# Kernel tuning notes

Measured on AMD Instinct MI355X. Metric: run time of the kernel, lower is better.

Reference implementation:

```python
import jax, jax.numpy as jnp
import numpy as np

B, SQ, SK, TT, DM, H, HKV, D, FF = 1, 2048, 3072, 4096, 2048, 16, 8, 128, 6144
EPS = 1e-6
THETA = 1000000.0

def rmsnorm(x, w):
    v = jnp.mean(x * x, axis=-1, keepdims=True)
    return x * jax.lax.rsqrt(v + EPS) * w

def rope_cos_sin(pos):
    inv = 1.0 / (THETA ** (jnp.arange(0, D, 2, dtype=jnp.float32) / D))
    f = pos.astype(jnp.float32)[..., None] * inv  # [B,S,D/2]
    emb = jnp.concatenate([f, f], axis=-1)        # [B,S,D]
    return jnp.cos(emb), jnp.sin(emb)

def rotate_half(x):
    x1, x2 = jnp.split(x, 2, axis=-1)
    return jnp.concatenate([-x2, x1], axis=-1)

def apply_rope(x, cos, sin):  # x: [B,H,S,D]; cos/sin: [B,S,D]
    return x * cos[:, None] + rotate_half(x) * sin[:, None]

def setup_inputs() -> dict:
    ks = jax.random.split(jax.random.key(0), 16)
    p = lambda i, sh: jax.random.normal(ks[i], sh, jnp.float32) * 0.02
    sri = lambda i, sh, mx: jnp.sort(jax.random.randint(ks[i], sh, 0, mx))
    return dict(
        hidden_states=jax.random.normal(ks[0], (B, SQ, DM), jnp.float32),
        kv_hidden=jax.random.normal(ks[1], (B, SK, DM), jnp.float32),
        causal_mask=jax.random.normal(ks[2], (B, 1, TT, TT), jnp.float32),
        w_q=p(3, (DM, H * D)), w_k=p(4, (DM, HKV * D)), w_v=p(5, (DM, HKV * D)),
        w_o=p(6, (H * D, DM)),
        q_norm_w=jnp.ones((D,), jnp.float32), k_norm_w=jnp.ones((D,), jnp.float32),
        ln1_w=jnp.ones((DM,), jnp.float32), ln2_w=jnp.ones((DM,), jnp.float32),
        w_gate=p(7, (DM, FF)), w_up=p(8, (DM, FF)), w_down=p(9, (FF, DM)),
        positions=sri(10, (B, SQ), TT), kv_positions=sri(11, (B, SK), TT),
        hs_idxs=sri(12, (SQ,), TT), key_idxs=sri(13, (SK,), TT))

def reference(hidden_states, kv_hidden, causal_mask, w_q, w_k, w_v, w_o,
              q_norm_w, k_norm_w, ln1_w, ln2_w, w_gate, w_up, w_down,
              positions, kv_positions, hs_idxs, key_idxs):
    # irregular mask reconstruction: gather kv dim then query dim (dims 3 then 2)
    mask = causal_mask[:, :, :, key_idxs][:, :, hs_idxs, :]  # [B,1,SQ,SK]
    # input_layernorm (RMSNorm)
    h = rmsnorm(hidden_states, ln1_w)
    hk = rmsnorm(kv_hidden, ln1_w)
    # Qwen3 attention: proj + per-head RMSNorm on q/k + RoPE + GQA
    q = rmsnorm((h @ w_q).reshape(B, SQ, H, D), q_norm_w).transpose(0, 2, 1, 3)
    k = rmsnorm((hk @ w_k).reshape(B, SK, HKV, D), k_norm_w).transpose(0, 2, 1, 3)
    v = (hk @ w_v).reshape(B, SK, HKV, D).transpose(0, 2, 1, 3)
    cq, sq = rope_cos_sin(positions)
    ck, sk = rope_cos_sin(kv_positions)
    q = apply_rope(q, cq, sq)
    k = apply_rope(k, ck, sk)
    rep = H // HKV
    k = jnp.repeat(k, rep, axis=1)
    v = jnp.repeat(v, rep, axis=1)
    scores = jnp.einsum('bhqd,bhkd->bhqk', q, k) * (D ** -0.5) + mask
    attn = jax.nn.softmax(scores, axis=-1)
    ctx = jnp.einsum('bhqk,bhkd->bhqd', attn, v).transpose(0, 2, 1, 3).reshape(B, SQ, H * D)
    hidden = hidden_states + ctx @ w_o
    # post-attention RMSNorm + SwiGLU MLP
    h2 = rmsnorm(hidden, ln2_w)
    mlp = (jax.nn.silu(h2 @ w_gate) * (h2 @ w_up)) @ w_down
    return hidden + mlp
```

## Files before the change

### kernel.cpp

```cpp
#include <hip/hip_runtime.h>
#include <math.h>

constexpr int SQ = 2048, SK = 3072, TT = 4096, DM = 2048;
constexpr int H = 16, HKV = 8, D = 128, FF = 6144;
#define EPS 1e-6f

typedef __attribute__((ext_vector_type(8))) short short8;
typedef __attribute__((ext_vector_type(4))) float f32x4;

#define GLOBAL_AS __attribute__((address_space(1)))
#define LDS_AS __attribute__((address_space(3)))

__device__ __forceinline__ unsigned short f2bf(float f) {
  unsigned u = __float_as_uint(f);
  unsigned r = (u + 0x7fffu + ((u >> 16) & 1u)) >> 16;
  return (unsigned short)r;
}
__device__ __forceinline__ float bflo(unsigned w) { return __uint_as_float(w << 16); }
__device__ __forceinline__ float bfhi(unsigned w) { return __uint_as_float(w & 0xffff0000u); }

__global__ __launch_bounds__(256) void wt_bf16_kernel(
    const float* __restrict__ w, unsigned short* __restrict__ wT, int K, int N) {
  __shared__ unsigned short s[64][73];
  int n0 = blockIdx.x * 64, k0 = blockIdx.y * 64;
  int tid = threadIdx.x;
  int cn = (tid & 15) * 4, rk = tid >> 4;
#pragma unroll
  for (int p = 0; p < 4; p++) {
    int k = rk + p * 16;
    const float4 f = *(const float4*)&w[(size_t)(k0 + k) * N + n0 + cn];
    s[k][cn] = f2bf(f.x); s[k][cn + 1] = f2bf(f.y);
    s[k][cn + 2] = f2bf(f.z); s[k][cn + 3] = f2bf(f.w);
  }
  __syncthreads();
  int ck = (tid & 15) * 4, rn = tid >> 4;
#pragma unroll
  for (int p = 0; p < 4; p++) {
    int n = rn + p * 16;
    ushort4 o;
    o.x = s[ck][n]; o.y = s[ck + 1][n]; o.z = s[ck + 2][n]; o.w = s[ck + 3][n];
    *(ushort4*)&wT[(size_t)(n0 + n) * K + k0 + ck] = o;
  }
}

__global__ __launch_bounds__(256) void vtrans_kernel(
    const float* __restrict__ vb, int ldv, unsigned short* __restrict__ vt) {
  __shared__ unsigned short s[64][72];
  int kv0 = blockIdx.x * 64, d0 = blockIdx.y * 64, kvh = blockIdx.z;
  int tid = threadIdx.x;
  int cd = (tid & 15) * 4, rk = tid >> 4;
#pragma unroll
  for (int p = 0; p < 4; p++) {
    int kv = rk + p * 16;
    const float4 f = *(const float4*)&vb[(size_t)(kv0 + kv) * ldv + kvh * D + d0 + cd];
    s[kv][cd] = f2bf(f.x); s[kv][cd + 1] = f2bf(f.y);
    s[kv][cd + 2] = f2bf(f.z); s[kv][cd + 3] = f2bf(f.w);
  }
  __syncthreads();
  int ck = (tid & 15) * 4, rd = tid >> 4;
#pragma unroll
  for (int p = 0; p < 4; p++) {
    int d = rd + p * 16;
    ushort4 o;
    o.x = s[ck][d]; o.y = s[ck + 1][d]; o.z = s[ck + 2][d]; o.w = s[ck + 3][d];
    *(ushort4*)&vt[((size_t)kvh * D + d0 + d) * SK + kv0 + ck] = o;
  }
}

__global__ __launch_bounds__(256) void rmsnorm_bf16_kernel(
    const float* __restrict__ x, const float* __restrict__ w,
    unsigned short* __restrict__ y) {
  int row = blockIdx.x;
  const float* xr = x + (size_t)row * DM;
  int c = threadIdx.x * 8;
  float4 a = *(const float4*)&xr[c];
  float4 b = *(const float4*)&xr[c + 4];
  float ss = a.x * a.x + a.y * a.y + a.z * a.z + a.w * a.w +
             b.x * b.x + b.y * b.y + b.z * b.z + b.w * b.w;
  for (int o = 32; o > 0; o >>= 1) ss += __shfl_down(ss, o);
  __shared__ float sred[4];
  int lane = threadIdx.x & 63, wid = threadIdx.x >> 6;
  if (lane == 0) sred[wid] = ss;
  __syncthreads();
  if (threadIdx.x == 0)
    sred[0] = rsqrtf((sred[0] + sred[1] + sred[2] + sred[3]) * (1.0f / (float)DM) + EPS);
  __syncthreads();
  float sc = sred[0];
  float4 wa = *(const float4*)&w[c];
  float4 wb = *(const float4*)&w[c + 4];
  ushort4 o1, o2;
  o1.x = f2bf(a.x * sc * wa.x); o1.y = f2bf(a.y * sc * wa.y);
  o1.z = f2bf(a.z * sc * wa.z); o1.w = f2bf(a.w * sc * wa.w);
  o2.x = f2bf(b.x * sc * wb.x); o2.y = f2bf(b.y * sc * wb.y);
  o2.z = f2bf(b.z * sc * wb.z); o2.w = f2bf(b.w * sc * wb.w);
  unsigned short* yr = y + (size_t)row * DM + c;
  *(ushort4*)&yr[0] = o1;
  *(ushort4*)&yr[4] = o2;
}

template <bool OUTBF>
__global__ __launch_bounds__(256) void mgemm_kernel(
    const unsigned short* __restrict__ A, const unsigned short* __restrict__ BT1,
    const unsigned short* __restrict__ BT2, int N1,
    void* __restrict__ C1p, void* __restrict__ C2p, int ld1, int ld2,
    int M, int N, int K) {
  __shared__ unsigned short As[128 * 64];
  __shared__ unsigned short Bs[128 * 64];
  const int tid = threadIdx.x;
  const int wave = tid >> 6, lane = tid & 63;
  const int bm = blockIdx.y * 128, bn = blockIdx.x * 128;
  const bool second = bn >= N1;
  const unsigned short* BT = second ? BT2 : BT1;
  const int bnl = second ? bn - N1 : bn;
  void* Cp = second ? C2p : C1p;
  const int ldc = second ? ld2 : ld1;
  const int wr = wave >> 1, wc = wave & 1;
  const int fl = lane & 15, fk = lane >> 4;

  const int srow = wave * 8 + (lane >> 3);
  const int schunk = (lane & 7) ^ (srow & 7);
  const unsigned short* Abase = A + (size_t)(bm + srow) * K + schunk * 8;
  const unsigned short* Bbase = BT + (size_t)(bnl + srow) * K + schunk * 8;

  f32x4 acc[4][4];
#pragma unroll
  for (int m = 0; m < 4; m++)
#pragma unroll
    for (int n = 0; n < 4; n++)
#pragma unroll
      for (int e = 0; e < 4; e++) acc[m][n][e] = 0.f;

  for (int k0 = 0; k0 < K; k0 += 64) {
#pragma unroll
    for (int p = 0; p < 4; p++) {
      __builtin_amdgcn_global_load_lds(
          (GLOBAL_AS unsigned*)(Abase + (size_t)(p * 32) * K + k0),
          (LDS_AS unsigned*)&As[(p * 32 + wave * 8) * 64], 16, 0, 0);
      __builtin_amdgcn_global_load_lds(
          (GLOBAL_AS unsigned*)(Bbase + (size_t)(p * 32) * K + k0),
          (LDS_AS unsigned*)&Bs[(p * 32 + wave * 8) * 64], 16, 0, 0);
    }
    __syncthreads();
#pragma unroll
    for (int kk = 0; kk < 2; kk++) {
      short8 a_[4], b_[4];
#pragma unroll
      for (int m = 0; m < 4; m++) {
        int row = wr * 64 + m * 16 + fl;
        int ch = (kk * 4 + fk) ^ (row & 7);
        a_[m] = *(const short8*)&As[row * 64 + ch * 8];
      }
#pragma unroll
      for (int n = 0; n < 4; n++) {
        int row = wc * 64 + n * 16 + fl;
        int ch = (kk * 4 + fk) ^ (row & 7);
        b_[n] = *(const short8*)&Bs[row * 64 + ch * 8];
      }
#pragma unroll
      for (int m = 0; m < 4; m++)
#pragma unroll
        for (int n = 0; n < 4; n++)
          acc[m][n] = __builtin_amdgcn_mfma_f32_16x16x32_bf16(
              a_[m], b_[n], acc[m][n], 0, 0, 0);
    }
    __syncthreads();
  }

#pragma unroll
  for (int m = 0; m < 4; m++) {
    int row0 = bm + wr * 64 + m * 16 + fk * 4;
#pragma unroll
    for (int n = 0; n < 4; n++) {
      int col = bnl + wc * 64 + n * 16 + fl;
#pragma unroll
      for (int r = 0; r < 4; r++) {
        size_t idx = (size_t)(row0 + r) * ldc + col;
        float v = acc[m][n][r];
        if (OUTBF) ((unsigned short*)Cp)[idx] = f2bf(v);
        else ((float*)Cp)[idx] = v;
      }
    }
  }
}

__global__ __launch_bounds__(256) void msplit_kernel(
    const unsigned short* __restrict__ A, const unsigned short* __restrict__ BT,
    float* __restrict__ C, int M, int N, int K, int kchunk) {
  __shared__ unsigned short As[128 * 64];
  __shared__ unsigned short Bs[128 * 64];
  const int tid = threadIdx.x;
  const int wave = tid >> 6, lane = tid & 63;
  const int bm = blockIdx.y * 128, bn = blockIdx.x * 128;
  const int kbeg = blockIdx.z * kchunk, kend = kbeg + kchunk;
  const int wr = wave >> 1, wc = wave & 1;
  const int fl = lane & 15, fk = lane >> 4;

  const int srow = wave * 8 + (lane >> 3);
  const int schunk = (lane & 7) ^ (srow & 7);
  const unsigned short* Abase = A + (size_t)(bm + srow) * K + schunk * 8;
  const unsigned short* Bbase = BT + (size_t)(bn + srow) * K + schunk * 8;

  f32x4 acc[4][4];
#pragma unroll
  for (int m = 0; m < 4; m++)
#pragma unroll
    for (int n = 0; n < 4; n++)
#pragma unroll
      for (int e = 0; e < 4; e++) acc[m][n][e] = 0.f;

  for (int k0 = kbeg; k0 < kend; k0 += 64) {
#pragma unroll
    for (int p = 0; p < 4; p++) {
      __builtin_amdgcn_global_load_lds(
          (GLOBAL_AS unsigned*)(Abase + (size_t)(p * 32) * K + k0),
          (LDS_AS unsigned*)&As[(p * 32 + wave * 8) * 64], 16, 0, 0);
      __builtin_amdgcn_global_load_lds(
          (GLOBAL_AS unsigned*)(Bbase + (size_t)(p * 32) * K + k0),
          (LDS_AS unsigned*)&Bs[(p * 32 + wave * 8) * 64], 16, 0, 0);
    }
    __syncthreads();
#pragma unroll
    for (int kk = 0; kk < 2; kk++) {
      short8 a_[4], b_[4];
#pragma unroll
      for (int m = 0; m < 4; m++) {
        int row = wr * 64 + m * 16 + fl;
        int ch = (kk * 4 + fk) ^ (row & 7);
        a_[m] = *(const short8*)&As[row * 64 + ch * 8];
      }
#pragma unroll
      for (int n = 0; n < 4; n++) {
        int row = wc * 64 + n * 16 + fl;
        int ch = (kk * 4 + fk) ^ (row & 7);
        b_[n] = *(const short8*)&Bs[row * 64 + ch * 8];
      }
#pragma unroll
      for (int m = 0; m < 4; m++)
#pragma unroll
        for (int n = 0; n < 4; n++)
          acc[m][n] = __builtin_amdgcn_mfma_f32_16x16x32_bf16(
              a_[m], b_[n], acc[m][n], 0, 0, 0);
    }
    __syncthreads();
  }

#pragma unroll
  for (int m = 0; m < 4; m++) {
    int row0 = bm + wr * 64 + m * 16 + fk * 4;
#pragma unroll
    for (int n = 0; n < 4; n++) {
      int col = bn + wc * 64 + n * 16 + fl;
#pragma unroll
      for (int r = 0; r < 4; r++)
        unsafeAtomicAdd(&C[(size_t)(row0 + r) * N + col], acc[m][n][r]);
    }
  }
}

__global__ __launch_bounds__(256) void zero4_kernel(float4* __restrict__ p, int n4) {
  int i = blockIdx.x * 256 + threadIdx.x;
  if (i < n4) p[i] = make_float4(0.f, 0.f, 0.f, 0.f);
}
__global__ __launch_bounds__(256) void copy4_kernel(
    float4* __restrict__ d, const float4* __restrict__ s, int n4) {
  int i = blockIdx.x * 256 + threadIdx.x;
  if (i < n4) d[i] = s[i];
}

__global__ __launch_bounds__(128) void qknorm_rope_bf16_kernel(
    const float* __restrict__ x, int ldx, const float* __restrict__ nw,
    const int* __restrict__ pos, unsigned short* __restrict__ out, int S) {
  int s = blockIdx.x, hh = blockIdx.y;
  const float* xr = x + (size_t)s * ldx + hh * D;
  int d = threadIdx.x;
  float vv = xr[d];
  float ss = vv * vv;
  for (int o = 32; o > 0; o >>= 1) ss += __shfl_down(ss, o);
  __shared__ float sred[2];
  __shared__ float sn[D];
  if ((d & 63) == 0) sred[d >> 6] = ss;
  __syncthreads();
  float ms = (sred[0] + sred[1]) * (1.0f / (float)D);
  float n = vv * rsqrtf(ms + EPS) * nw[d];
  sn[d] = n;
  __syncthreads();
  int t = d & 63;
  float inv = powf(1000000.0f, -((float)(2 * t)) / (float)D);
  float ang = (float)pos[s] * inv;
  float c = cosf(ang), si = sinf(ang);
  float rh = (d < 64) ? -sn[d + 64] : sn[d - 64];
  out[((size_t)hh * S + s) * D + d] = f2bf(n * c + rh * si);
}

__global__ __launch_bounds__(256) void mask_gather_kernel(
    const float* __restrict__ mask, const int* __restrict__ hs_idxs,
    const int* __restrict__ key_idxs, float* __restrict__ maskg) {
  int q = blockIdx.x;
  const float* base = mask + (size_t)hs_idxs[q] * TT;
  float* out = maskg + (size_t)q * SK;
  for (int j = threadIdx.x; j < SK; j += 256) out[j] = base[key_idxs[j]];
}

__global__ __launch_bounds__(256) void attn_mfma_kernel(
    const unsigned short* __restrict__ qbf, const unsigned short* __restrict__ kbf,
    const unsigned short* __restrict__ vtbf, const float* __restrict__ maskg,
    unsigned short* __restrict__ ctx) {
  __shared__ unsigned short Ks[2][64 * 128];
  __shared__ unsigned short Vts[2][128 * 64];
  __shared__ unsigned short Pl[4][16 * 72];

  const int tid = threadIdx.x;
  const int wave = tid >> 6, lane = tid & 63;
  const int fl = lane & 15, g = lane >> 4;
  const float scale = 0.08838834764831845f;

  int bid = blockIdx.x;
  int swz = (bid & 7) * 64 + (bid >> 3);
  const int hh = swz >> 5;
  const int qblk = (swz & 31) * 64;
  const int kvh = hh >> 1;

  short8 qf[4];
  {
    const unsigned short* qrow = qbf + ((size_t)hh * SQ + qblk + wave * 16 + fl) * D;
#pragma unroll
    for (int kw = 0; kw < 4; kw++) qf[kw] = *(const short8*)&qrow[kw * 32 + g * 8];
  }

  const unsigned short* ksrc[4];
  const unsigned short* vsrc[4];
  {
    int krow = lane >> 4;
    int vrow = lane >> 3;
    int vcs = (lane & 7) ^ vrow;
#pragma unroll
    for (int p = 0; p < 4; p++) {
      int rowk = wave * 16 + p * 4 + krow;
      int kcs = (lane & 15) ^ (rowk & 7);
      ksrc[p] = kbf + ((size_t)kvh * SK + rowk) * D + kcs * 8;
      int rowv = wave * 32 + p * 8 + vrow;
      vsrc[p] = vtbf + ((size_t)kvh * D + rowv) * SK + vcs * 8;
    }
  }
  const float* mbase = maskg + (size_t)(qblk + wave * 16 + fl) * SK + g * 4;

  float m_i = -INFINITY, l_i = 0.f;
  f32x4 o[8];
#pragma unroll
  for (int n = 0; n < 8; n++)
#pragma unroll
    for (int r = 0; r < 4; r++) o[n][r] = 0.f;

#define STAGE(bufi)                                                            \
  {                                                                            \
    _Pragma("unroll")                                                          \
    for (int p = 0; p < 4; p++) {                                              \
      __builtin_amdgcn_global_load_lds(                                        \
          (GLOBAL_AS unsigned*)ksrc[p],                                        \
          (LDS_AS unsigned*)&Ks[bufi][(wave * 16 + p * 4) * 128], 16, 0, 0);   \
      __builtin_amdgcn_global_load_lds(                                        \
          (GLOBAL_AS unsigned*)vsrc[p],                                        \
          (LDS_AS unsigned*)&Vts[bufi][(wave * 32 + p * 8) * 64], 16, 0, 0);   \
      ksrc[p] += 64 * D;                                                       \
      vsrc[p] += 64;                                                           \
    }                                                                          \
  }

  STAGE(0);
  __syncthreads();

  const int NT = SK / 64;
  for (int t = 0; t < NT; t++) {
    const int buf = t & 1;
    if (t + 1 < NT) STAGE(buf ^ 1);

    float4 mv[4];
#pragma unroll
    for (int kvf = 0; kvf < 4; kvf++) mv[kvf] = *(const float4*)(mbase + kvf * 16);
    mbase += 64;

    f32x4 sa[4];
#pragma unroll
    for (int kvf = 0; kvf < 4; kvf++)
#pragma unroll
      for (int r = 0; r < 4; r++) sa[kvf][r] = 0.f;
#pragma unroll
    for (int kw = 0; kw < 4; kw++) {
#pragma unroll
      for (int kvf = 0; kvf < 4; kvf++) {
        int row = kvf * 16 + fl;
        int ch = (kw * 4 + g) ^ (fl & 7);
        short8 kf = *(const short8*)&Ks[buf][row * 128 + ch * 8];
        sa[kvf] = __builtin_amdgcn_mfma_f32_16x16x32_bf16(kf, qf[kw], sa[kvf], 0, 0, 0);
      }
    }

    float p4[4][4];
    float rm = -INFINITY;
#pragma unroll
    for (int kvf = 0; kvf < 4; kvf++) {
      p4[kvf][0] = sa[kvf][0] * scale + mv[kvf].x;
      p4[kvf][1] = sa[kvf][1] * scale + mv[kvf].y;
      p4[kvf][2] = sa[kvf][2] * scale + mv[kvf].z;
      p4[kvf][3] = sa[kvf][3] * scale + mv[kvf].w;
#pragma unroll
      for (int r = 0; r < 4; r++) rm = fmaxf(rm, p4[kvf][r]);
    }
    rm = fmaxf(rm, __shfl_xor(rm, 16));
    rm = fmaxf(rm, __shfl_xor(rm, 32));
    const int need = __any(rm > m_i + 8.f);
    float mn = need ? fmaxf(m_i, rm) : m_i;
    float alpha = need ? __expf(m_i - mn) : 1.f;
    m_i = mn;
    float rs = 0.f;
#pragma unroll
    for (int kvf = 0; kvf < 4; kvf++) {
#pragma unroll
      for (int r = 0; r < 4; r++) { p4[kvf][r] = __expf(p4[kvf][r] - mn); rs += p4[kvf][r]; }
      ushort4 pk;
      pk.x = f2bf(p4[kvf][0]); pk.y = f2bf(p4[kvf][1]);
      pk.z = f2bf(p4[kvf][2]); pk.w = f2bf(p4[kvf][3]);
      *(ushort4*)&Pl[wave][fl * 72 + kvf * 16 + g * 4] = pk;
    }
    rs += __shfl_xor(rs, 16);
    rs += __shfl_xor(rs, 32);
    l_i = l_i * alpha + rs;

    if (need) {
      float av[4];
#pragma unroll
      for (int r = 0; r < 4; r++) av[r] = __shfl(alpha, 4 * g + r);
#pragma unroll
      for (int n = 0; n < 8; n++)
#pragma unroll
        for (int r = 0; r < 4; r++) o[n][r] *= av[r];
    }

#pragma unroll
    for (int k = 0; k < 2; k++) {
      short8 pf = *(const short8*)&Pl[wave][fl * 72 + k * 32 + g * 8];
#pragma unroll
      for (int n = 0; n < 8; n++) {
        int row = n * 16 + fl;
        int ch = (k * 4 + g) ^ (fl & 7);
        short8 vf = *(const short8*)&Vts[buf][row * 64 + ch * 8];
        o[n] = __builtin_amdgcn_mfma_f32_16x16x32_bf16(pf, vf, o[n], 0, 0, 0);
      }
    }
    __syncthreads();
  }

#pragma unroll
  for (int r = 0; r < 4; r++) {
    float linv = 1.f / __shfl(l_i, 4 * g + r);
    size_t base = ((size_t)(qblk + wave * 16 + 4 * g + r)) * (H * D) + (size_t)hh * D + fl;
#pragma unroll
    for (int n = 0; n < 8; n++) ctx[base + n * 16] = f2bf(o[n][r] * linv);
  }
#undef STAGE
}

__device__ __forceinline__ unsigned silu2(unsigned gw, unsigned uw) {
  float g0 = bflo(gw), g1 = bfhi(gw), u0 = bflo(uw), u1 = bfhi(uw);
  float r0 = g0 / (1.f + __expf(-g0)) * u0;
  float r1 = g1 / (1.f + __expf(-g1)) * u1;
  return ((unsigned)f2bf(r1) << 16) | f2bf(r0);
}
__global__ __launch_bounds__(256) void silu_mul_bf16_kernel(
    unsigned short* __restrict__ g, const unsigned short* __restrict__ u, int n8) {
  int i = blockIdx.x * 256 + threadIdx.x;
  if (i >= n8) return;
  uint4 G = *(const uint4*)&g[(size_t)i * 8];
  uint4 U = *(const uint4*)&u[(size_t)i * 8];
  G.x = silu2(G.x, U.x); G.y = silu2(G.y, U.y);
  G.z = silu2(G.z, U.z); G.w = silu2(G.w, U.w);
  *(uint4*)&g[(size_t)i * 8] = G;
}

extern "C" void kernel_launch(void* const* d_in, const int* in_sizes, int n_in,
                              void* d_out, int out_size, void* d_ws, size_t ws_size,
                              hipStream_t stream) {
  (void)in_sizes; (void)n_in; (void)out_size; (void)ws_size;
  const float* hidden_states = (const float*)d_in[0];
  const float* kv_hidden     = (const float*)d_in[1];
  const float* causal_mask   = (const float*)d_in[2];
  const float* w_q      = (const float*)d_in[3];
  const float* w_k      = (const float*)d_in[4];
  const float* w_v      = (const float*)d_in[5];
  const float* w_o      = (const float*)d_in[6];
  const float* q_norm_w = (const float*)d_in[7];
  const float* k_norm_w = (const float*)d_in[8];
  const float* ln1_w    = (const float*)d_in[9];
  const float* ln2_w    = (const float*)d_in[10];
  const float* w_gate   = (const float*)d_in[11];
  const float* w_up     = (const float*)d_in[12];
  const float* w_down   = (const float*)d_in[13];
  const int* positions    = (const int*)d_in[14];
  const int* kv_positions = (const int*)d_in[15];
  const int* hs_idxs      = (const int*)d_in[16];
  const int* key_idxs     = (const int*)d_in[17];

  char* wsb = (char*)d_ws;
  float* maskg           = (float*)(wsb + 0);
  unsigned short* h_bf   = (unsigned short*)(wsb + 25165824);
  unsigned short* hk_bf  = (unsigned short*)(wsb + 33554432);
  unsigned short* Wq     = (unsigned short*)(wsb + 46137344);
  unsigned short* Wkv    = (unsigned short*)(wsb + 54525952);
  float* qb              = (float*)(wsb + 62914560);
  float* kvb             = (float*)(wsb + 79691776);
  unsigned short* qbf    = (unsigned short*)(wsb + 104857600);
  unsigned short* kbf    = (unsigned short*)(wsb + 113246208);
  unsigned short* vtbf   = (unsigned short*)(wsb + 119537664);
  unsigned short* ctx_bf = (unsigned short*)(wsb + 125829120);
  float* hidden          = qb;
  unsigned short* Wo     = Wq;
  unsigned short* h2_bf  = h_bf;
  unsigned short* Wg     = (unsigned short*)(wsb + 0);
  unsigned short* Wu     = (unsigned short*)(wsb + 79691776);
  unsigned short* gate_bf = (unsigned short*)(wsb + 104857600);
  unsigned short* up_bf  = (unsigned short*)(wsb + 33554432);
  unsigned short* Wd     = (unsigned short*)(wsb + 33554432);

  mask_gather_kernel<<<SQ, 256, 0, stream>>>(causal_mask, hs_idxs, key_idxs, maskg);
  rmsnorm_bf16_kernel<<<SQ, 256, 0, stream>>>(hidden_states, ln1_w, h_bf);
  rmsnorm_bf16_kernel<<<SK, 256, 0, stream>>>(kv_hidden, ln1_w, hk_bf);

  wt_bf16_kernel<<<dim3((H * D) / 64, DM / 64), 256, 0, stream>>>(w_q, Wq, DM, H * D);
  wt_bf16_kernel<<<dim3((HKV * D) / 64, DM / 64), 256, 0, stream>>>(w_k, Wkv, DM, HKV * D);
  wt_bf16_kernel<<<dim3((HKV * D) / 64, DM / 64), 256, 0, stream>>>(
      w_v, Wkv + (size_t)(HKV * D) * DM, DM, HKV * D);

  zero4_kernel<<<(SQ * H * D / 4 + 255) / 256, 256, 0, stream>>>((float4*)qb, SQ * H * D / 4);
  msplit_kernel<<<dim3((H * D) / 128, SQ / 128, 2), 256, 0, stream>>>(
      h_bf, Wq, qb, SQ, H * D, DM, DM / 2);
  mgemm_kernel<false><<<dim3((2 * HKV * D) / 128, SK / 128), 256, 0, stream>>>(
      hk_bf, Wkv, nullptr, 2 * HKV * D, kvb, nullptr, 2 * HKV * D, 0, SK, 2 * HKV * D, DM);

  qknorm_rope_bf16_kernel<<<dim3(SQ, H), 128, 0, stream>>>(
      qb, H * D, q_norm_w, positions, qbf, SQ);
  qknorm_rope_bf16_kernel<<<dim3(SK, HKV), 128, 0, stream>>>(
      kvb, 2 * HKV * D, k_norm_w, kv_positions, kbf, SK);
  vtrans_kernel<<<dim3(SK / 64, D / 64, HKV), 256, 0, stream>>>(
      kvb + HKV * D, 2 * HKV * D, vtbf);

  attn_mfma_kernel<<<512, 256, 0, stream>>>(qbf, kbf, vtbf, maskg, ctx_bf);

  copy4_kernel<<<(SQ * DM / 4 + 255) / 256, 256, 0, stream>>>(
      (float4*)hidden, (const float4*)hidden_states, SQ * DM / 4);
  wt_bf16_kernel<<<dim3(DM / 64, (H * D) / 64), 256, 0, stream>>>(w_o, Wo, H * D, DM);
  msplit_kernel<<<dim3(DM / 128, SQ / 128, 2), 256, 0, stream>>>(
      ctx_bf, Wo, hidden, SQ, DM, H * D, (H * D) / 2);

  rmsnorm_bf16_kernel<<<SQ, 256, 0, stream>>>(hidden, ln2_w, h2_bf);
  wt_bf16_kernel<<<dim3(FF / 64, DM / 64), 256, 0, stream>>>(w_gate, Wg, DM, FF);
  wt_bf16_kernel<<<dim3(FF / 64, DM / 64), 256, 0, stream>>>(w_up, Wu, DM, FF);
  mgemm_kernel<true><<<dim3((2 * FF) / 128, SQ / 128), 256, 0, stream>>>(
      h2_bf, Wg, Wu, FF, gate_bf, up_bf, FF, FF, SQ, 2 * FF, DM);
  silu_mul_bf16_kernel<<<(SQ * FF / 8 + 255) / 256, 256, 0, stream>>>(
      gate_bf, up_bf, SQ * FF / 8);

  wt_bf16_kernel<<<dim3(DM / 64, FF / 64), 256, 0, stream>>>(w_down, Wd, FF, DM);
  copy4_kernel<<<(SQ * DM / 4 + 255) / 256, 256, 0, stream>>>(
      (float4*)d_out, (const float4*)hidden, SQ * DM / 4);
  msplit_kernel<<<dim3(DM / 128, SQ / 128, 3), 256, 0, stream>>>(
      gate_bf, Wd, (float*)d_out, SQ, DM, FF, FF / 3);
}
```

Before: 873.7 us.

## Process 32 query rows per wave in attention and split-K the KV projection

Each attention wave now handles two 16-row query tiles, so every K and V fragment read from LDS feeds two MFMAs. The grid shrinks from 512 to 256 blocks of 128 queries, and the P buffer gets an XOR-swizzled layout. The KV projection also switches from a plain GEMM to the split-K msplit kernel, with a zeroing pass added first. The attention change halves the number of blocks on a large GPU and raises register pressure (two sets of accumulators), which may reduce occupancy.

```diff
diff --git a/kernel.cpp b/kernel.cpp
--- a/kernel.cpp
+++ b/kernel.cpp
@@ -307,7 +307,7 @@
     unsigned short* __restrict__ ctx) {
   __shared__ unsigned short Ks[2][64 * 128];
   __shared__ unsigned short Vts[2][128 * 64];
-  __shared__ unsigned short Pl[4][16 * 72];
+  __shared__ unsigned short Pl[4][32 * 64];
 
   const int tid = threadIdx.x;
   const int wave = tid >> 6, lane = tid & 63;
@@ -315,16 +315,18 @@
   const float scale = 0.08838834764831845f;
 
   int bid = blockIdx.x;
-  int swz = (bid & 7) * 64 + (bid >> 3);
-  const int hh = swz >> 5;
-  const int qblk = (swz & 31) * 64;
+  int swz = (bid & 7) * 32 + (bid >> 3);
+  const int hh = swz >> 4;
+  const int qblk = (swz & 15) * 128;
   const int kvh = hh >> 1;
 
-  short8 qf[4];
-  {
-    const unsigned short* qrow = qbf + ((size_t)hh * SQ + qblk + wave * 16 + fl) * D;
-#pragma unroll
-    for (int kw = 0; kw < 4; kw++) qf[kw] = *(const short8*)&qrow[kw * 32 + g * 8];
+  short8 qf[2][4];
+#pragma unroll
+  for (int qi = 0; qi < 2; qi++) {
+    const unsigned short* qrow =
+        qbf + ((size_t)hh * SQ + qblk + wave * 32 + qi * 16 + fl) * D;
+#pragma unroll
+    for (int kw = 0; kw < 4; kw++) qf[qi][kw] = *(const short8*)&qrow[kw * 32 + g * 8];
   }
 
   const unsigned short* ksrc[4];
@@ -342,14 +344,17 @@
       vsrc[p] = vtbf + ((size_t)kvh * D + rowv) * SK + vcs * 8;
     }
   }
-  const float* mbase = maskg + (size_t)(qblk + wave * 16 + fl) * SK + g * 4;
-
-  float m_i = -INFINITY, l_i = 0.f;
-  f32x4 o[8];
-#pragma unroll
-  for (int n = 0; n < 8; n++)
-#pragma unroll
-    for (int r = 0; r < 4; r++) o[n][r] = 0.f;
+  const float* mbase0 = maskg + (size_t)(qblk + wave * 32 + fl) * SK + g * 4;
+  const float* mbase1 = mbase0 + (size_t)16 * SK;
+
+  float m_i[2] = {-INFINITY, -INFINITY}, l_i[2] = {0.f, 0.f};
+  f32x4 o[2][8];
+#pragma unroll
+  for (int mq = 0; mq < 2; mq++)
+#pragma unroll
+    for (int n = 0; n < 8; n++)
+#pragma unroll
+      for (int r = 0; r < 4; r++) o[mq][n][r] = 0.f;
 
 #define STAGE(bufi)                                                            \
   {                                                                            \
@@ -374,16 +379,21 @@
     const int buf = t & 1;
     if (t + 1 < NT) STAGE(buf ^ 1);
 
-    float4 mv[4];
-#pragma unroll
-    for (int kvf = 0; kvf < 4; kvf++) mv[kvf] = *(const float4*)(mbase + kvf * 16);
-    mbase += 64;
-
-    f32x4 sa[4];
-#pragma unroll
-    for (int kvf = 0; kvf < 4; kvf++)
-#pragma unroll
-      for (int r = 0; r < 4; r++) sa[kvf][r] = 0.f;
+    float4 mv[2][4];
+#pragma unroll
+    for (int kvf = 0; kvf < 4; kvf++) {
+      mv[0][kvf] = *(const float4*)(mbase0 + kvf * 16);
+      mv[1][kvf] = *(const float4*)(mbase1 + kvf * 16);
+    }
+    mbase0 += 64; mbase1 += 64;
+
+    f32x4 sa[2][4];
+#pragma unroll
+    for (int qi = 0; qi < 2; qi++)
+#pragma unroll
+      for (int kvf = 0; kvf < 4; kvf++)
+#pragma unroll
+        for (int r = 0; r < 4; r++) sa[qi][kvf][r] = 0.f;
 #pragma unroll
     for (int kw = 0; kw < 4; kw++) {
 #pragma unroll
@@ -391,71 +401,87 @@
         int row = kvf * 16 + fl;
         int ch = (kw * 4 + g) ^ (fl & 7);
         short8 kf = *(const short8*)&Ks[buf][row * 128 + ch * 8];
-        sa[kvf] = __builtin_amdgcn_mfma_f32_16x16x32_bf16(kf, qf[kw], sa[kvf], 0, 0, 0);
-      }
-    }
-
-    float p4[4][4];
-    float rm = -INFINITY;
-#pragma unroll
-    for (int kvf = 0; kvf < 4; kvf++) {
-      p4[kvf][0] = sa[kvf][0] * scale + mv[kvf].x;
-      p4[kvf][1] = sa[kvf][1] * scale + mv[kvf].y;
-      p4[kvf][2] = sa[kvf][2] * scale + mv[kvf].z;
-      p4[kvf][3] = sa[kvf][3] * scale + mv[kvf].w;
-#pragma unroll
-      for (int r = 0; r < 4; r++) rm = fmaxf(rm, p4[kvf][r]);
-    }
-    rm = fmaxf(rm, __shfl_xor(rm, 16));
-    rm = fmaxf(rm, __shfl_xor(rm, 32));
-    const int need = __any(rm > m_i + 8.f);
-    float mn = need ? fmaxf(m_i, rm) : m_i;
-    float alpha = need ? __expf(m_i - mn) : 1.f;
-    m_i = mn;
-    float rs = 0.f;
-#pragma unroll
-    for (int kvf = 0; kvf < 4; kvf++) {
-#pragma unroll
-      for (int r = 0; r < 4; r++) { p4[kvf][r] = __expf(p4[kvf][r] - mn); rs += p4[kvf][r]; }
-      ushort4 pk;
-      pk.x = f2bf(p4[kvf][0]); pk.y = f2bf(p4[kvf][1]);
-      pk.z = f2bf(p4[kvf][2]); pk.w = f2bf(p4[kvf][3]);
-      *(ushort4*)&Pl[wave][fl * 72 + kvf * 16 + g * 4] = pk;
-    }
-    rs += __shfl_xor(rs, 16);
-    rs += __shfl_xor(rs, 32);
-    l_i = l_i * alpha + rs;
-
-    if (need) {
-      float av[4];
-#pragma unroll
-      for (int r = 0; r < 4; r++) av[r] = __shfl(alpha, 4 * g + r);
-#pragma unroll
-      for (int n = 0; n < 8; n++)
-#pragma unroll
-        for (int r = 0; r < 4; r++) o[n][r] *= av[r];
+        sa[0][kvf] = __builtin_amdgcn_mfma_f32_16x16x32_bf16(kf, qf[0][kw], sa[0][kvf], 0, 0, 0);
+        sa[1][kvf] = __builtin_amdgcn_mfma_f32_16x16x32_bf16(kf, qf[1][kw], sa[1][kvf], 0, 0, 0);
+      }
+    }
+
+#pragma unroll
+    for (int qi = 0; qi < 2; qi++) {
+      const int ql = qi * 16 + fl;
+      float p4[4][4];
+      float rm = -INFINITY;
+#pragma unroll
+      for (int kvf = 0; kvf < 4; kvf++) {
+        p4[kvf][0] = sa[qi][kvf][0] * scale + mv[qi][kvf].x;
+        p4[kvf][1] = sa[qi][kvf][1] * scale + mv[qi][kvf].y;
+        p4[kvf][2] = sa[qi][kvf][2] * scale + mv[qi][kvf].z;
+        p4[kvf][3] = sa[qi][kvf][3] * scale + mv[qi][kvf].w;
+#pragma unroll
+        for (int r = 0; r < 4; r++) rm = fmaxf(rm, p4[kvf][r]);
+      }
+      rm = fmaxf(rm, __shfl_xor(rm, 16));
+      rm = fmaxf(rm, __shfl_xor(rm, 32));
+      const int need = __any(rm > m_i[qi] + 8.f);
+      float mn = need ? fmaxf(m_i[qi], rm) : m_i[qi];
+      float alpha = need ? __expf(m_i[qi] - mn) : 1.f;
+      m_i[qi] = mn;
+      float rs = 0.f;
+#pragma unroll
+      for (int kvf = 0; kvf < 4; kvf++) {
+#pragma unroll
+        for (int r = 0; r < 4; r++) { p4[kvf][r] = __expf(p4[kvf][r] - mn); rs += p4[kvf][r]; }
+        ushort4 pk;
+        pk.x = f2bf(p4[kvf][0]); pk.y = f2bf(p4[kvf][1]);
+        pk.z = f2bf(p4[kvf][2]); pk.w = f2bf(p4[kvf][3]);
+        int pp = (kvf * 2 + (g >> 1)) ^ (ql & 7);
+        *(ushort4*)&Pl[wave][ql * 64 + pp * 8 + (g & 1) * 4] = pk;
+      }
+      rs += __shfl_xor(rs, 16);
+      rs += __shfl_xor(rs, 32);
+      l_i[qi] = l_i[qi] * alpha + rs;
+
+      if (need) {
+        float av[4];
+#pragma unroll
+        for (int r = 0; r < 4; r++) av[r] = __shfl(alpha, 4 * g + r);
+#pragma unroll
+        for (int n = 0; n < 8; n++)
+#pragma unroll
+          for (int r = 0; r < 4; r++) o[qi][n][r] *= av[r];
+      }
     }
 
 #pragma unroll
     for (int k = 0; k < 2; k++) {
-      short8 pf = *(const short8*)&Pl[wave][fl * 72 + k * 32 + g * 8];
+      short8 pf0, pf1;
+      {
+        int pp0 = (k * 4 + g) ^ (fl & 7);
+        pf0 = *(const short8*)&Pl[wave][fl * 64 + pp0 * 8];
+        pf1 = *(const short8*)&Pl[wave][(16 + fl) * 64 + pp0 * 8];
+      }
 #pragma unroll
       for (int n = 0; n < 8; n++) {
         int row = n * 16 + fl;
         int ch = (k * 4 + g) ^ (fl & 7);
         short8 vf = *(const short8*)&Vts[buf][row * 64 + ch * 8];
-        o[n] = __builtin_amdgcn_mfma_f32_16x16x32_bf16(pf, vf, o[n], 0, 0, 0);
+        o[0][n] = __builtin_amdgcn_mfma_f32_16x16x32_bf16(pf0, vf, o[0][n], 0, 0, 0);
+        o[1][n] = __builtin_amdgcn_mfma_f32_16x16x32_bf16(pf1, vf, o[1][n], 0, 0, 0);
       }
     }
     __syncthreads();
   }
 
 #pragma unroll
-  for (int r = 0; r < 4; r++) {
-    float linv = 1.f / __shfl(l_i, 4 * g + r);
-    size_t base = ((size_t)(qblk + wave * 16 + 4 * g + r)) * (H * D) + (size_t)hh * D + fl;
-#pragma unroll
-    for (int n = 0; n < 8; n++) ctx[base + n * 16] = f2bf(o[n][r] * linv);
+  for (int mq = 0; mq < 2; mq++) {
+#pragma unroll
+    for (int r = 0; r < 4; r++) {
+      float linv = 1.f / __shfl(l_i[mq], 4 * g + r);
+      size_t base = ((size_t)(qblk + wave * 32 + mq * 16 + 4 * g + r)) * (H * D) +
+                    (size_t)hh * D + fl;
+#pragma unroll
+      for (int n = 0; n < 8; n++) ctx[base + n * 16] = f2bf(o[mq][n][r] * linv);
+    }
   }
 #undef STAGE
 }
@@ -531,10 +557,12 @@
       w_v, Wkv + (size_t)(HKV * D) * DM, DM, HKV * D);
 
   zero4_kernel<<<(SQ * H * D / 4 + 255) / 256, 256, 0, stream>>>((float4*)qb, SQ * H * D / 4);
+  zero4_kernel<<<(SK * 2 * HKV * D / 4 + 255) / 256, 256, 0, stream>>>(
+      (float4*)kvb, SK * 2 * HKV * D / 4);
   msplit_kernel<<<dim3((H * D) / 128, SQ / 128, 2), 256, 0, stream>>>(
       h_bf, Wq, qb, SQ, H * D, DM, DM / 2);
-  mgemm_kernel<false><<<dim3((2 * HKV * D) / 128, SK / 128), 256, 0, stream>>>(
-      hk_bf, Wkv, nullptr, 2 * HKV * D, kvb, nullptr, 2 * HKV * D, 0, SK, 2 * HKV * D, DM);
+  msplit_kernel<<<dim3((2 * HKV * D) / 128, SK / 128, 2), 256, 0, stream>>>(
+      hk_bf, Wkv, kvb, SK, 2 * HKV * D, DM, DM / 2);
 
   qknorm_rope_bf16_kernel<<<dim3(SQ, H), 128, 0, stream>>>(
       qb, H * D, q_norm_w, positions, qbf, SQ);
@@ -543,7 +571,7 @@
   vtrans_kernel<<<dim3(SK / 64, D / 64, HKV), 256, 0, stream>>>(
       kvb + HKV * D, 2 * HKV * D, vtbf);
 
-  attn_mfma_kernel<<<512, 256, 0, stream>>>(qbf, kbf, vtbf, maskg, ctx_bf);
+  attn_mfma_kernel<<<256, 256, 0, stream>>>(qbf, kbf, vtbf, maskg, ctx_bf);
 
   copy4_kernel<<<(SQ * DM / 4 + 255) / 256, 256, 0, stream>>>(
       (float4*)hidden, (const float4*)hidden_states, SQ * DM / 4);
```

After: 924.9 us. +5.9%, slower.
